# Performance work log

Measured on AMD Instinct MI355X. Metric: run time of the kernel, lower is better.

Reference implementation:

```python
import jax, jax.numpy as jnp
import numpy as np

N = 100000
IN_C = 256
OUT_C = 256
E = 500000


def gcn_conv(x, W, b, edges):
    """PyG GCNConv: add self-loops, symmetric D^-1/2 (A+I) D^-1/2 normalization,
    then scatter-add of transformed source features into targets, plus bias."""
    n = x.shape[0]
    loop = jnp.arange(n, dtype=edges.dtype)
    row = jnp.concatenate([edges[0], loop])  # source
    col = jnp.concatenate([edges[1], loop])  # target
    deg = jax.ops.segment_sum(jnp.ones_like(col, dtype=x.dtype), col, num_segments=n)
    dis = jax.lax.rsqrt(deg)  # deg >= 1 after self-loops
    norm = dis[row] * dis[col]  # [E+n]
    h = x @ W  # [n, out]
    msg = h[row] * norm[:, None]  # gather + scale
    return jax.ops.segment_sum(msg, col, num_segments=n) + b


def setup_inputs() -> dict:
    key = jax.random.key(0)
    ks = jax.random.split(key, 24)
    x = jax.random.normal(ks[0], (N, IN_C), dtype=jnp.float32)
    edges00 = jax.random.randint(ks[1], (2, E), 0, N, dtype=jnp.int32)
    edges01 = jax.random.randint(ks[2], (2, E), 0, N, dtype=jnp.int32)
    edges10 = jax.random.randint(ks[3], (2, E), 0, N, dtype=jnp.int32)
    edges11 = jax.random.randint(ks[4], (2, E), 0, N, dtype=jnp.int32)
    t0 = (jax.random.uniform(ks[5], (N,)) > 0.5).astype(jnp.float32)
    t1 = 1.0 - t0
    scale = 1.0 / np.sqrt(IN_C)
    W1 = jax.random.normal(ks[6], (IN_C, OUT_C), dtype=jnp.float32) * scale
    W2 = jax.random.normal(ks[7], (IN_C, OUT_C), dtype=jnp.float32) * scale
    W3 = jax.random.normal(ks[8], (IN_C, OUT_C), dtype=jnp.float32) * scale
    W4 = jax.random.normal(ks[9], (IN_C, OUT_C), dtype=jnp.float32) * scale
    b1 = jnp.zeros((OUT_C,), jnp.float32)
    b2 = jnp.zeros((OUT_C,), jnp.float32)
    b3 = jnp.zeros((OUT_C,), jnp.float32)
    b4 = jnp.zeros((OUT_C,), jnp.float32)
    p0 = jax.random.normal(ks[10], (OUT_C,), dtype=jnp.float32)
    p1 = jax.random.normal(ks[11], (OUT_C,), dtype=jnp.float32)
    p2 = jax.random.normal(ks[12], (OUT_C,), dtype=jnp.float32)
    p3 = jax.random.normal(ks[13], (OUT_C,), dtype=jnp.float32)
    p4 = jax.random.normal(ks[14], (OUT_C,), dtype=jnp.float32)
    p5 = jax.random.normal(ks[15], (OUT_C,), dtype=jnp.float32)
    return dict(x=x, edges00=edges00, edges01=edges01, edges10=edges10, edges11=edges11,
                type0_idx=t0, type1_idx=t1,
                W1=W1, b1=b1, W2=W2, b2=b2, W3=W3, b3=b3, W4=W4, b4=b4,
                p0=p0, p1=p1, p2=p2, p3=p3, p4=p4, p5=p5)


def reference(x, edges00, edges01, edges10, edges11, type0_idx, type1_idx,
              W1, b1, W2, b2, W3, b3, W4, b4, p0, p1, p2, p3, p4, p5):
    # x0/x1: first feature column masked by node type, broadcast over out channels
    x0c = type0_idx * x[:, 0]  # [N]
    x1c = type1_idx * x[:, 0]
    x00 = gcn_conv(x, W1, b1, edges00)
    x01 = gcn_conv(x, W2, b2, edges01)
    x10 = gcn_conv(x, W3, b3, edges10)
    x11 = gcn_conv(x, W4, b4, edges11)
    out = (x0c[:, None] * p0 + x1c[:, None] * p1
           + x00 * p2 + x01 * p3 + x10 * p4 + x11 * p5)
    return out
```

## Files before the change

### kernel.cpp

```cpp
#include <hip/hip_runtime.h>


#define PCAP 24

typedef __bf16 v8bf __attribute__((ext_vector_type(8)));
typedef float v4f __attribute__((ext_vector_type(4)));

__device__ __forceinline__ unsigned short f2bf(float f) {
  unsigned u = __float_as_uint(f);
  u += 0x7fffu + ((u >> 16) & 1u);
  return (unsigned short)(u >> 16);
}
__device__ __forceinline__ float bf2f(unsigned short s) {
  return __uint_as_float(((unsigned)s) << 16);
}
__device__ __forceinline__ void async_ld16(const void* g, void* l) {
  __builtin_amdgcn_global_load_lds((__attribute__((address_space(1))) void*)g,
                                   (__attribute__((address_space(3))) void*)l,
                                   16, 0, 0);
}

__global__ void lc_zero(int* __restrict__ p, int n) {
  int i = blockIdx.x * 256 + threadIdx.x;
  if (i < n) p[i] = 0;
}

__global__ void lc_fill(const int* __restrict__ e0, const int* __restrict__ e1,
                        const int* __restrict__ e2, const int* __restrict__ e3,
                        int* __restrict__ cursor, unsigned* __restrict__ payload,
                        int N, int E) {
  int e = blockIdx.x * 256 + threadIdx.x;
  if (e >= E) return;
  int k = blockIdx.y;
  const int* ed = (k == 0) ? e0 : (k == 1) ? e1 : (k == 2) ? e2 : e3;
  int src = ed[e], col = ed[E + e];
  int idx = k * N + col;
  int pos = atomicAdd(&cursor[idx], 1);
  if (pos < PCAP) payload[(size_t)idx * PCAP + pos] = (unsigned)src;
}

__global__ void lc_dis(const int* __restrict__ deg, float* __restrict__ dis, int M) {
  int i = blockIdx.x * 256 + threadIdx.x;
  if (i < M) dis[i] = rsqrtf((float)(deg[i] + 1));
}

__global__ void lc_pack(unsigned* __restrict__ payload, const int* __restrict__ deg,
                        const float* __restrict__ dis, int N) {
  int i = blockIdx.x * 256 + threadIdx.x;
  if (i >= N * PCAP) return;
  int k = blockIdx.y;
  int col = i / PCAP, slot = i - col * PCAP;
  int list = k * N + col;
  int cnt = deg[list];
  if (cnt > PCAP) cnt = PCAP;
  if (slot >= cnt) return;
  size_t pidx = (size_t)list * PCAP + slot;
  unsigned src = payload[pidx];
  float ds = dis[(size_t)k * N + src];
  unsigned q = (unsigned)(ds * 32767.0f + 0.5f);
  payload[pidx] = (q << 17) | src;
}

__global__ void lc_prep(const float* __restrict__ W1, const float* __restrict__ W2,
                        const float* __restrict__ W3, const float* __restrict__ W4,
                        const float* __restrict__ b1, const float* __restrict__ b2,
                        const float* __restrict__ b3, const float* __restrict__ b4,
                        const float* __restrict__ p2, const float* __restrict__ p3,
                        const float* __restrict__ p4, const float* __restrict__ p5,
                        unsigned short* __restrict__ Wt, float* __restrict__ biasc) {
  int b = blockIdx.x;
  int k = b >> 8, co = b & 255;
  int kk = threadIdx.x;
  const float* W = (k == 0) ? W1 : (k == 1) ? W2 : (k == 2) ? W3 : W4;
  const float* p = (k == 0) ? p2 : (k == 1) ? p3 : (k == 2) ? p4 : p5;
  Wt[(size_t)co * 1024 + k * 256 + kk] = f2bf(W[kk * 256 + co] * p[co]);
  if (b == 0) {
    int c = kk;
    biasc[c] = b1[c] * p2[c] + b2[c] * p3[c] + b3[c] * p4[c] + b4[c] * p5[c];
  }
}

__global__ void lc_cvt(const float4* __restrict__ x4, ushort4* __restrict__ xb4,
                       const float* __restrict__ t0, const float* __restrict__ t1,
                       float* __restrict__ m0, float* __restrict__ m1, int n4) {
  int i = blockIdx.x * 256 + threadIdx.x;
  if (i >= n4) return;
  float4 v = x4[i];
  ushort4 r;
  r.x = f2bf(v.x); r.y = f2bf(v.y); r.z = f2bf(v.z); r.w = f2bf(v.w);
  xb4[i] = r;
  if ((i & 63) == 0) {
    int n = i >> 6;
    float xc = v.x;
    m0[n] = t0[n] * xc;
    m1[n] = t1[n] * xc;
  }
}

__global__ __launch_bounds__(256) void lc_aggx(
    const unsigned short* __restrict__ xb, unsigned short* __restrict__ Agg,
    int aggw, int kcount, int kbase, const int* __restrict__ deg,
    const float* __restrict__ dis, const unsigned* __restrict__ payload, int N) {
  int t = threadIdx.x;
  int w = t >> 6, lane = t & 63;
  int n, k, koff;
  if (kcount == 4) { n = blockIdx.x; k = w; koff = k * 256; }
  else { n = blockIdx.x * 4 + w; k = kbase; koff = 0; }
  if (n >= N) return;
  int c = lane * 4;
  int idx = k * N + n;

  float dn = dis[idx];
  float dns = dn * (1.0f / 32767.0f);
  float s = dn * dn;
  ushort4 hv = *(const ushort4*)&xb[(size_t)n * 256 + c];
  float a0 = bf2f(hv.x) * s, a1 = bf2f(hv.y) * s;
  float a2 = bf2f(hv.z) * s, a3 = bf2f(hv.w) * s;

  size_t start = (size_t)idx * PCAP;
  int cnt = deg[idx];
  if (cnt > PCAP) cnt = PCAP;
  int i = 0;
  for (; i + 4 <= cnt; i += 4) {
    unsigned p0v = payload[start + i];
    unsigned p1v = payload[start + i + 1];
    unsigned p2v = payload[start + i + 2];
    unsigned p3v = payload[start + i + 3];
    unsigned s0 = p0v & 0x1FFFFu, s1 = p1v & 0x1FFFFu;
    unsigned s2 = p2v & 0x1FFFFu, s3 = p3v & 0x1FFFFu;
    ushort4 g0 = *(const ushort4*)&xb[(size_t)s0 * 256 + c];
    ushort4 g1 = *(const ushort4*)&xb[(size_t)s1 * 256 + c];
    ushort4 g2 = *(const ushort4*)&xb[(size_t)s2 * 256 + c];
    ushort4 g3 = *(const ushort4*)&xb[(size_t)s3 * 256 + c];
    float n0 = (float)(p0v >> 17) * dns, n1 = (float)(p1v >> 17) * dns;
    float n2 = (float)(p2v >> 17) * dns, n3 = (float)(p3v >> 17) * dns;
    a0 += bf2f(g0.x) * n0 + bf2f(g1.x) * n1 + bf2f(g2.x) * n2 + bf2f(g3.x) * n3;
    a1 += bf2f(g0.y) * n0 + bf2f(g1.y) * n1 + bf2f(g2.y) * n2 + bf2f(g3.y) * n3;
    a2 += bf2f(g0.z) * n0 + bf2f(g1.z) * n1 + bf2f(g2.z) * n2 + bf2f(g3.z) * n3;
    a3 += bf2f(g0.w) * n0 + bf2f(g1.w) * n1 + bf2f(g2.w) * n2 + bf2f(g3.w) * n3;
  }
  for (; i < cnt; i++) {
    unsigned p0v = payload[start + i];
    unsigned s0 = p0v & 0x1FFFFu;
    ushort4 g0 = *(const ushort4*)&xb[(size_t)s0 * 256 + c];
    float n0 = (float)(p0v >> 17) * dns;
    a0 += bf2f(g0.x) * n0;
    a1 += bf2f(g0.y) * n0;
    a2 += bf2f(g0.z) * n0;
    a3 += bf2f(g0.w) * n0;
  }
  ushort4 r;
  r.x = f2bf(a0); r.y = f2bf(a1); r.z = f2bf(a2); r.w = f2bf(a3);
  *(ushort4*)&Agg[(size_t)n * aggw + koff + c] = r;
}

__global__ __launch_bounds__(512) void lc_gemm(
    const unsigned short* __restrict__ A, int strideA,
    const unsigned short* __restrict__ B, int strideB, int K,
    float* __restrict__ out, int Mrows, int addprev, int doepi,
    const float* __restrict__ m0, const float* __restrict__ m1,
    const float* __restrict__ p0, const float* __restrict__ p1,
    const float* __restrict__ biasc) {
  __shared__ alignas(16) unsigned short As[128 * 32];
  __shared__ alignas(16) unsigned short Bs[256 * 32];
  int t = threadIdx.x;
  int w = t >> 6, lane = t & 63;
  int wm = w & 1, wn = w >> 1;
  int quad = lane >> 4, l16 = lane & 15;
  int row0 = blockIdx.x * 128;

  v4f acc[4][4];
#pragma unroll
  for (int mt = 0; mt < 4; mt++)
#pragma unroll
    for (int nt = 0; nt < 4; nt++) {
      v4f z = {0.f, 0.f, 0.f, 0.f};
      acc[mt][nt] = z;
    }

  const int ra = t >> 2;
  const int e0 = (t & 3) * 8;
  const int sws = (ra & 3) << 3;
  const unsigned swf = (unsigned)((l16 & 3) << 3);

  for (int kk = 0; kk < K; kk += 32) {
    {
      int grow = row0 + ra;
      if (grow >= Mrows) grow = Mrows - 1;
      async_ld16(A + (size_t)grow * strideA + kk + (e0 ^ sws), &As[ra * 32 + e0]);
      async_ld16(B + (size_t)ra * strideB + kk + (e0 ^ sws), &Bs[ra * 32 + e0]);
      async_ld16(B + (size_t)(128 + ra) * strideB + kk + (e0 ^ sws),
                 &Bs[(128 + ra) * 32 + e0]);
    }
    __syncthreads();

    v8bf af[4], bfr[4];
    unsigned eq = ((unsigned)(quad * 8)) ^ swf;
#pragma unroll
    for (int mt = 0; mt < 4; mt++) {
      int r = wm * 64 + mt * 16 + l16;
      af[mt] = *(const v8bf*)&As[(unsigned)r * 32 + eq];
    }
#pragma unroll
    for (int nt = 0; nt < 4; nt++) {
      int n = wn * 64 + nt * 16 + l16;
      bfr[nt] = *(const v8bf*)&Bs[(unsigned)n * 32 + eq];
    }
#pragma unroll
    for (int mt = 0; mt < 4; mt++)
#pragma unroll
      for (int nt = 0; nt < 4; nt++)
        acc[mt][nt] =
            __builtin_amdgcn_mfma_f32_16x16x32_bf16(af[mt], bfr[nt], acc[mt][nt], 0, 0, 0);
    __syncthreads();
  }

  float pc0[4], pc1[4], bc[4];
#pragma unroll
  for (int nt = 0; nt < 4; nt++) {
    int gcol = wn * 64 + nt * 16 + l16;
    pc0[nt] = doepi ? p0[gcol] : 0.f;
    pc1[nt] = doepi ? p1[gcol] : 0.f;
    bc[nt] = doepi ? biasc[gcol] : 0.f;
  }
#pragma unroll
  for (int mt = 0; mt < 4; mt++)
#pragma unroll
    for (int r = 0; r < 4; r++) {
      int grow = row0 + wm * 64 + mt * 16 + quad * 4 + r;
      if (grow >= Mrows) continue;
      float m0v = 0.f, m1v = 0.f;
      if (doepi) { m0v = m0[grow]; m1v = m1[grow]; }
#pragma unroll
      for (int nt = 0; nt < 4; nt++) {
        int gcol = wn * 64 + nt * 16 + l16;
        size_t o = (size_t)grow * 256 + gcol;
        float v = acc[mt][nt][r];
        if (addprev) v += out[o];
        if (doepi) v += m0v * pc0[nt] + m1v * pc1[nt] + bc[nt];
        out[o] = v;
      }
    }
}

extern "C" void kernel_launch(void* const* d_in, const int* in_sizes, int n_in,
                              void* d_out, int out_size, void* d_ws, size_t ws_size,
                              hipStream_t stream) {
  const float* x = (const float*)d_in[0];
  const int* e00 = (const int*)d_in[1];
  const int* e01 = (const int*)d_in[2];
  const int* e10 = (const int*)d_in[3];
  const int* e11 = (const int*)d_in[4];
  const float* t0 = (const float*)d_in[5];
  const float* t1 = (const float*)d_in[6];
  const float* W1 = (const float*)d_in[7];
  const float* b1 = (const float*)d_in[8];
  const float* W2 = (const float*)d_in[9];
  const float* b2 = (const float*)d_in[10];
  const float* W3 = (const float*)d_in[11];
  const float* b3 = (const float*)d_in[12];
  const float* W4 = (const float*)d_in[13];
  const float* b4 = (const float*)d_in[14];
  const float* p0 = (const float*)d_in[15];
  const float* p1 = (const float*)d_in[16];
  const float* p2 = (const float*)d_in[17];
  const float* p3 = (const float*)d_in[18];
  const float* p4 = (const float*)d_in[19];
  const float* p5 = (const float*)d_in[20];
  float* out = (float*)d_out;

  int N = in_sizes[0] / 256;
  int E = in_sizes[1] / 2;
  int M4 = 4 * N;

  char* wp = (char*)d_ws;
  auto carve = [&](size_t bytes) {
    void* r = (void*)wp;
    wp += (bytes + 255) & ~(size_t)255;
    return r;
  };
  unsigned short* xb = (unsigned short*)carve((size_t)N * 256 * 2);
  unsigned short* Wt = (unsigned short*)carve((size_t)256 * 1024 * 2);
  int* cursor = (int*)carve((size_t)M4 * 4);
  float* dis = (float*)carve((size_t)M4 * 4);
  float* biasc = (float*)carve(256 * 4);
  float* m0 = (float*)carve((size_t)N * 4);
  float* m1 = (float*)carve((size_t)N * 4);
  unsigned* payload = (unsigned*)carve((size_t)M4 * PCAP * 4);
  size_t used = (size_t)(wp - (char*)d_ws);
  size_t remain = (ws_size > used) ? ws_size - used : 0;
  bool fat = remain >= (size_t)N * 1024 * 2;
  unsigned short* Agg = (unsigned short*)wp;

  int gE = (E + 255) / 256;
  int gM = (M4 + 255) / 256;
  int gP = (N * PCAP + 255) / 256;

  lc_zero<<<gM, 256, 0, stream>>>(cursor, M4);
  lc_fill<<<dim3(gE, 4), 256, 0, stream>>>(e00, e01, e10, e11, cursor, payload, N, E);
  lc_dis<<<gM, 256, 0, stream>>>(cursor, dis, M4);
  lc_pack<<<dim3(gP, 4), 256, 0, stream>>>(payload, cursor, dis, N);
  lc_prep<<<1024, 256, 0, stream>>>(W1, W2, W3, W4, b1, b2, b3, b4,
                                    p2, p3, p4, p5, Wt, biasc);
  lc_cvt<<<(N * 64 + 255) / 256, 256, 0, stream>>>((const float4*)x, (ushort4*)xb,
                                                   t0, t1, m0, m1, N * 64);

  int gemm_mb = (N + 127) / 128;
  if (fat) {
    lc_aggx<<<N, 256, 0, stream>>>(xb, Agg, 1024, 4, 0, cursor, dis, payload, N);
    lc_gemm<<<gemm_mb, 512, 0, stream>>>(Agg, 1024, Wt, 1024, 1024, out, N,
                                         0, 1, m0, m1, p0, p1, biasc);
  } else {
    for (int k = 0; k < 4; k++) {
      lc_aggx<<<(N + 3) / 4, 256, 0, stream>>>(xb, Agg, 256, 1, k, cursor, dis,
                                               payload, N);
      lc_gemm<<<gemm_mb, 512, 0, stream>>>(Agg, 256, Wt + k * 256, 1024, 256,
                                           out, N, (k > 0) ? 1 : 0,
                                           (k == 3) ? 1 : 0, m0, m1, p0, p1,
                                           biasc);
    }
  }
}
```

Baseline: 707.3 us.

## Double-buffer GEMM LDS loads, fold rsqrt into consumers, tile weight prep

The GEMM now double-buffers its A/B LDS tiles, so the next k-slice's async global-to-LDS loads are issued before the current MFMAs, and it uses one barrier per iteration instead of two. The separate dis kernel and buffer are removed, with rsqrt(deg+1) recomputed inline in pack and aggregation. The zero kernel is replaced with hipMemsetAsync, and the weight transpose/prep kernel now goes through a shared-memory tile and writes vectorized stores. Together these cut launches and overlap memory traffic with compute, at the cost of twice the GEMM LDS, which may lower occupancy.

Result: no change. 700.0 us (-1.0%).

```diff
diff --git a/kernel.cpp b/kernel.cpp
--- a/kernel.cpp
+++ b/kernel.cpp
@@ -18,11 +18,6 @@
   __builtin_amdgcn_global_load_lds((__attribute__((address_space(1))) void*)g,
                                    (__attribute__((address_space(3))) void*)l,
                                    16, 0, 0);
-}
-
-__global__ void lc_zero(int* __restrict__ p, int n) {
-  int i = blockIdx.x * 256 + threadIdx.x;
-  if (i < n) p[i] = 0;
 }
 
 __global__ void lc_fill(const int* __restrict__ e0, const int* __restrict__ e1,
@@ -39,13 +34,8 @@
   if (pos < PCAP) payload[(size_t)idx * PCAP + pos] = (unsigned)src;
 }
 
-__global__ void lc_dis(const int* __restrict__ deg, float* __restrict__ dis, int M) {
-  int i = blockIdx.x * 256 + threadIdx.x;
-  if (i < M) dis[i] = rsqrtf((float)(deg[i] + 1));
-}
-
 __global__ void lc_pack(unsigned* __restrict__ payload, const int* __restrict__ deg,
-                        const float* __restrict__ dis, int N) {
+                        int N) {
   int i = blockIdx.x * 256 + threadIdx.x;
   if (i >= N * PCAP) return;
   int k = blockIdx.y;
@@ -56,7 +46,7 @@
   if (slot >= cnt) return;
   size_t pidx = (size_t)list * PCAP + slot;
   unsigned src = payload[pidx];
-  float ds = dis[(size_t)k * N + src];
+  float ds = rsqrtf((float)(deg[(size_t)k * N + src] + 1));
   unsigned q = (unsigned)(ds * 32767.0f + 0.5f);
   payload[pidx] = (q << 17) | src;
 }
@@ -68,15 +58,39 @@
                         const float* __restrict__ p2, const float* __restrict__ p3,
                         const float* __restrict__ p4, const float* __restrict__ p5,
                         unsigned short* __restrict__ Wt, float* __restrict__ biasc) {
-  int b = blockIdx.x;
-  int k = b >> 8, co = b & 255;
-  int kk = threadIdx.x;
+  __shared__ float tile[256][33];
+  int k = blockIdx.y, co0 = blockIdx.x * 32;
+  int t = threadIdx.x;
   const float* W = (k == 0) ? W1 : (k == 1) ? W2 : (k == 2) ? W3 : W4;
   const float* p = (k == 0) ? p2 : (k == 1) ? p3 : (k == 2) ? p4 : p5;
-  Wt[(size_t)co * 1024 + k * 256 + kk] = f2bf(W[kk * 256 + co] * p[co]);
-  if (b == 0) {
-    int c = kk;
+
+  if (blockIdx.x == 0 && k == 0) {
+    int c = t;
     biasc[c] = b1[c] * p2[c] + b2[c] * p3[c] + b3[c] * p4[c] + b4[c] * p5[c];
+  }
+
+  int coL = t & 31, kkB = t >> 5;
+#pragma unroll 4
+  for (int pass = 0; pass < 32; ++pass) {
+    int kk = pass * 8 + kkB;
+    tile[kk][coL] = W[kk * 256 + co0 + coL];
+  }
+  __syncthreads();
+
+  int co = t >> 3, seg0 = t & 7;
+  float pv = p[co0 + co];
+#pragma unroll
+  for (int i = 0; i < 4; ++i) {
+    int s = seg0 + 8 * i;
+    ushort4 lo, hi;
+    int kk = s * 8;
+    lo.x = f2bf(tile[kk + 0][co] * pv); lo.y = f2bf(tile[kk + 1][co] * pv);
+    lo.z = f2bf(tile[kk + 2][co] * pv); lo.w = f2bf(tile[kk + 3][co] * pv);
+    hi.x = f2bf(tile[kk + 4][co] * pv); hi.y = f2bf(tile[kk + 5][co] * pv);
+    hi.z = f2bf(tile[kk + 6][co] * pv); hi.w = f2bf(tile[kk + 7][co] * pv);
+    unsigned short* dst = Wt + (size_t)(co0 + co) * 1024 + k * 256 + kk;
+    *(ushort4*)dst = lo;
+    *(ushort4*)(dst + 4) = hi;
   }
 }
 
@@ -100,7 +114,7 @@
 __global__ __launch_bounds__(256) void lc_aggx(
     const unsigned short* __restrict__ xb, unsigned short* __restrict__ Agg,
     int aggw, int kcount, int kbase, const int* __restrict__ deg,
-    const float* __restrict__ dis, const unsigned* __restrict__ payload, int N) {
+    const unsigned* __restrict__ payload, int N) {
   int t = threadIdx.x;
   int w = t >> 6, lane = t & 63;
   int n, k, koff;
@@ -110,7 +124,8 @@
   int c = lane * 4;
   int idx = k * N + n;
 
-  float dn = dis[idx];
+  int degv = deg[idx];
+  float dn = rsqrtf((float)(degv + 1));
   float dns = dn * (1.0f / 32767.0f);
   float s = dn * dn;
   ushort4 hv = *(const ushort4*)&xb[(size_t)n * 256 + c];
@@ -118,8 +133,7 @@
   float a2 = bf2f(hv.z) * s, a3 = bf2f(hv.w) * s;
 
   size_t start = (size_t)idx * PCAP;
-  int cnt = deg[idx];
-  if (cnt > PCAP) cnt = PCAP;
+  int cnt = (degv > PCAP) ? PCAP : degv;
   int i = 0;
   for (; i + 4 <= cnt; i += 4) {
     unsigned p0v = payload[start + i];
@@ -161,8 +175,8 @@
     const float* __restrict__ m0, const float* __restrict__ m1,
     const float* __restrict__ p0, const float* __restrict__ p1,
     const float* __restrict__ biasc) {
-  __shared__ alignas(16) unsigned short As[128 * 32];
-  __shared__ alignas(16) unsigned short Bs[256 * 32];
+  __shared__ alignas(16) unsigned short As[2][128 * 32];
+  __shared__ alignas(16) unsigned short Bs[2][256 * 32];
   int t = threadIdx.x;
   int w = t >> 6, lane = t & 63;
   int wm = w & 1, wn = w >> 1;
@@ -183,28 +197,39 @@
   const int sws = (ra & 3) << 3;
   const unsigned swf = (unsigned)((l16 & 3) << 3);
 
+  int growA = row0 + ra;
+  if (growA >= Mrows) growA = Mrows - 1;
+  const unsigned short* Ap = A + (size_t)growA * strideA + (e0 ^ sws);
+  const unsigned short* Bp0 = B + (size_t)ra * strideB + (e0 ^ sws);
+  const unsigned short* Bp1 = B + (size_t)(128 + ra) * strideB + (e0 ^ sws);
+  const int lA = ra * 32 + e0;
+  const int lB0 = ra * 32 + e0, lB1 = (128 + ra) * 32 + e0;
+
+  async_ld16(Ap, &As[0][lA]);
+  async_ld16(Bp0, &Bs[0][lB0]);
+  async_ld16(Bp1, &Bs[0][lB1]);
+  asm volatile("s_waitcnt vmcnt(0)" ::: "memory");
+  __builtin_amdgcn_s_barrier();
+
+  int cur = 0;
   for (int kk = 0; kk < K; kk += 32) {
-    {
-      int grow = row0 + ra;
-      if (grow >= Mrows) grow = Mrows - 1;
-      async_ld16(A + (size_t)grow * strideA + kk + (e0 ^ sws), &As[ra * 32 + e0]);
-      async_ld16(B + (size_t)ra * strideB + kk + (e0 ^ sws), &Bs[ra * 32 + e0]);
-      async_ld16(B + (size_t)(128 + ra) * strideB + kk + (e0 ^ sws),
-                 &Bs[(128 + ra) * 32 + e0]);
-    }
-    __syncthreads();
+    if (kk + 32 < K) {
+      async_ld16(Ap + kk + 32, &As[cur ^ 1][lA]);
+      async_ld16(Bp0 + kk + 32, &Bs[cur ^ 1][lB0]);
+      async_ld16(Bp1 + kk + 32, &Bs[cur ^ 1][lB1]);
+    }
 
     v8bf af[4], bfr[4];
     unsigned eq = ((unsigned)(quad * 8)) ^ swf;
 #pragma unroll
     for (int mt = 0; mt < 4; mt++) {
       int r = wm * 64 + mt * 16 + l16;
-      af[mt] = *(const v8bf*)&As[(unsigned)r * 32 + eq];
+      af[mt] = *(const v8bf*)&As[cur][(unsigned)r * 32 + eq];
     }
 #pragma unroll
     for (int nt = 0; nt < 4; nt++) {
       int n = wn * 64 + nt * 16 + l16;
-      bfr[nt] = *(const v8bf*)&Bs[(unsigned)n * 32 + eq];
+      bfr[nt] = *(const v8bf*)&Bs[cur][(unsigned)n * 32 + eq];
     }
 #pragma unroll
     for (int mt = 0; mt < 4; mt++)
@@ -212,7 +237,10 @@
       for (int nt = 0; nt < 4; nt++)
         acc[mt][nt] =
             __builtin_amdgcn_mfma_f32_16x16x32_bf16(af[mt], bfr[nt], acc[mt][nt], 0, 0, 0);
-    __syncthreads();
+
+    asm volatile("s_waitcnt vmcnt(0)" ::: "memory");
+    __builtin_amdgcn_s_barrier();
+    cur ^= 1;
   }
 
   float pc0[4], pc1[4], bc[4];
@@ -282,7 +310,6 @@
   unsigned short* xb = (unsigned short*)carve((size_t)N * 256 * 2);
   unsigned short* Wt = (unsigned short*)carve((size_t)256 * 1024 * 2);
   int* cursor = (int*)carve((size_t)M4 * 4);
-  float* dis = (float*)carve((size_t)M4 * 4);
   float* biasc = (float*)carve(256 * 4);
   float* m0 = (float*)carve((size_t)N * 4);
   float* m1 = (float*)carve((size_t)N * 4);
@@ -293,26 +320,24 @@
   unsigned short* Agg = (unsigned short*)wp;
 
   int gE = (E + 255) / 256;
-  int gM = (M4 + 255) / 256;
   int gP = (N * PCAP + 255) / 256;
 
-  lc_zero<<<gM, 256, 0, stream>>>(cursor, M4);
+  hipMemsetAsync(cursor, 0, (size_t)M4 * 4, stream);
   lc_fill<<<dim3(gE, 4), 256, 0, stream>>>(e00, e01, e10, e11, cursor, payload, N, E);
-  lc_dis<<<gM, 256, 0, stream>>>(cursor, dis, M4);
-  lc_pack<<<dim3(gP, 4), 256, 0, stream>>>(payload, cursor, dis, N);
-  lc_prep<<<1024, 256, 0, stream>>>(W1, W2, W3, W4, b1, b2, b3, b4,
-                                    p2, p3, p4, p5, Wt, biasc);
+  lc_pack<<<dim3(gP, 4), 256, 0, stream>>>(payload, cursor, N);
+  lc_prep<<<dim3(8, 4), 256, 0, stream>>>(W1, W2, W3, W4, b1, b2, b3, b4,
+                                          p2, p3, p4, p5, Wt, biasc);
   lc_cvt<<<(N * 64 + 255) / 256, 256, 0, stream>>>((const float4*)x, (ushort4*)xb,
                                                    t0, t1, m0, m1, N * 64);
 
   int gemm_mb = (N + 127) / 128;
   if (fat) {
-    lc_aggx<<<N, 256, 0, stream>>>(xb, Agg, 1024, 4, 0, cursor, dis, payload, N);
+    lc_aggx<<<N, 256, 0, stream>>>(xb, Agg, 1024, 4, 0, cursor, payload, N);
     lc_gemm<<<gemm_mb, 512, 0, stream>>>(Agg, 1024, Wt, 1024, 1024, out, N,
                                          0, 1, m0, m1, p0, p1, biasc);
   } else {
     for (int k = 0; k < 4; k++) {
-      lc_aggx<<<(N + 3) / 4, 256, 0, stream>>>(xb, Agg, 256, 1, k, cursor, dis,
+      lc_aggx<<<(N + 3) / 4, 256, 0, stream>>>(xb, Agg, 256, 1, k, cursor,
                                                payload, N);
       lc_gemm<<<gemm_mb, 512, 0, stream>>>(Agg, 256, Wt + k * 256, 1024, 256,
                                            out, N, (k > 0) ? 1 : 0,
```
